# Performance work log

Measured on AMD Instinct MI355X. Metric: run time of the kernel, lower is better.

The kernel has to match this reference:

```python
import jax, jax.numpy as jnp
import numpy as np

N_ROOMS = 126          # len(building.rooms)
N = 2 + N_ROOMS        # state dim (reset_iv: 2 + n_rooms)
M = 1 + N_ROOMS        # input dim u = [Tout, Q_watts...]
T = 200000             # number of eval times
DT = 30.0              # seconds between eval points
TOUT_DT = 3600.0       # outside-temp table grid spacing (s)
K = 1700               # table length (covers 1000 + T*DT seconds)
LOAD_MAX = 500.0       # physical_loads_scaling: W/m^2 upper bound


def setup_inputs() -> dict:
    key = jax.random.key(0)
    ks = jax.random.split(key, 6)
    # Stable RC-style state matrix: negative diagonal dominates
    A = 1e-5 * jax.random.normal(ks[0], (N, N), dtype=jnp.float32) - 2e-4 * jnp.eye(N, dtype=jnp.float32)
    B = 1e-6 * jax.random.normal(ks[1], (N, M), dtype=jnp.float32)
    loads = jax.random.normal(ks[2], (2, N_ROOMS), dtype=jnp.float32)   # raw params (pre-sigmoid)
    areas = 10.0 + 40.0 * jax.random.uniform(ks[3], (N_ROOMS,), dtype=jnp.float32)  # room areas m^2
    Tout_vals = 10.0 + 5.0 * jax.random.normal(ks[4], (K,), dtype=jnp.float32)      # hourly Tout table
    t_eval = 1000.0 + DT * jnp.arange(T, dtype=jnp.float32)
    iv = 26.0 * jnp.ones((N, 1), dtype=jnp.float32)
    return {"A": A, "B": B, "loads": loads, "areas": areas,
            "Tout_vals": Tout_vals, "t_eval": t_eval, "iv": iv, "action": 1}


def _interp_tout(vals, t):
    # linear interpolation on a uniform grid starting at t=0 (replaces scipy interp1d)
    pos = t / TOUT_DT
    idx = jnp.clip(jnp.floor(pos).astype(jnp.int32), 0, K - 2)
    w = pos - idx.astype(pos.dtype)
    return vals[idx] * (1.0 - w) + vals[idx + 1] * w


def reference(A, B, loads, areas, Tout_vals, t_eval, iv, action):
    t0 = t_eval[0]
    ts = t_eval - t0
    # _build_loads: sigmoid transform + physical scaling
    lp = jax.nn.sigmoid(loads) * LOAD_MAX
    cool_load, gain_load = lp[0], lp[1]
    # f_ode constants: Q_area = -cool*action + gain; Q_watts = proportional_heating
    Q_watts = (-cool_load * action + gain_load) * areas        # [n_rooms]
    b_q = B[:, 1:] @ Q_watts                                   # [N] constant forcing
    b_T = B[:, 0]                                              # [N] Tout coupling
    x0 = iv[:, 0]

    def f(t, x):
        Tout = _interp_tout(Tout_vals, t + t0)
        return A @ x + b_T * Tout + b_q

    # torchdiffeq method='rk4' -> rk4_alt_step_func (3/8 rule)
    def step(x, tt):
        t, tn = tt
        dt = tn - t
        k1 = f(t, x)
        k2 = f(t + dt / 3.0, x + dt * k1 / 3.0)
        k3 = f(t + dt * 2.0 / 3.0, x + dt * (k2 - k1 / 3.0))
        k4 = f(t + dt, x + dt * (k1 - k2 + k3))
        xn = x + dt * (k1 + 3.0 * (k2 + k3) + k4) / 8.0
        return xn, xn

    _, traj = jax.lax.scan(step, x0, (ts[:-1], ts[1:]))
    out = jnp.concatenate([x0[None, :], traj], axis=0)         # [T, N]
    return out[..., None]                                      # [T, N, 1] matching iv shape
```

## Files before the change

### kernel.cpp

```cpp
#include <hip/hip_runtime.h>

#define N 128
#define NR 126
#define MBCOL 127
#define TSTEPS 200000
#define L1 49
#define C1 4096
#define L2 64
#define C2 64
#define KT 1700

#define OFF_Z     0
#define OFF_S     16384
#define OFF_P     32768
#define OFF_PW2   65536
#define OFF_PW4   81920
#define OFF_PW8   98304
#define OFF_PW16  114688
#define OFF_PW32  131072
#define OFF_Q     147456
#define OFF_WC    180224
#define OFF_ACC   212992
#define OFF_DELTA 737280
#define OFF_BQ    745472
#define OFF_BST   753664
#define OFF_PEH   65536
#define OFF_PEL   75776

typedef float v4f __attribute__((ext_vector_type(4)));
typedef __attribute__((ext_vector_type(8))) short bf16x8;
typedef __attribute__((ext_vector_type(4))) float f32x4;

#define LBAR() do { \
  __builtin_amdgcn_sched_barrier(0); \
  asm volatile("s_waitcnt lgkmcnt(0)" ::: "memory"); \
  __builtin_amdgcn_sched_barrier(0); \
  __builtin_amdgcn_s_barrier(); \
  __builtin_amdgcn_sched_barrier(0); \
} while (0)

#define GLD4(dst, p) \
  asm volatile("global_load_dwordx4 %0, %1, off" : "=v"(dst) : "v"(p))
#define PINQ(q) \
  asm volatile("s_waitcnt vmcnt(0)" \
    : "+v"(q[0]),"+v"(q[1]),"+v"(q[2]),"+v"(q[3]), \
      "+v"(q[4]),"+v"(q[5]),"+v"(q[6]),"+v"(q[7]), \
      "+v"(q[8]),"+v"(q[9]),"+v"(q[10]),"+v"(q[11]), \
      "+v"(q[12]),"+v"(q[13]),"+v"(q[14]),"+v"(q[15]))

__device__ __forceinline__ void loadQ16(v4f* qv, const float* pb)
{
  #pragma unroll
  for (int s = 0; s < 16; ++s) GLD4(qv[s], pb + 4*s);
  PINQ(qv);
}

__device__ __forceinline__ void bsplit(float f, unsigned short& h, unsigned short& l)
{
  unsigned int u = __float_as_uint(f);
  unsigned int r = (u + 0x7FFFu + ((u >> 16) & 1u)) >> 16;
  float hf = __uint_as_float(r << 16);
  h = (unsigned short)r;
  float lo = f - hf;
  unsigned int u2 = __float_as_uint(lo);
  unsigned int r2 = (u2 + 0x7FFFu + ((u2 >> 16) & 1u)) >> 16;
  l = (unsigned short)r2;
}

__global__ __launch_bounds__(128) void kPrep(
    const float* __restrict__ A, const float* __restrict__ B,
    const float* __restrict__ loads, const float* __restrict__ areas,
    const float* __restrict__ iv, const int* __restrict__ action,
    float* __restrict__ ws, float* __restrict__ out)
{
  __shared__ float qw[NR];
  __shared__ float ys[4][N];
  __shared__ float qs[4][N];
  int t = threadIdx.x;
  float actf = (float)action[0];
  if (t < NR) {
    float lc = (1.0f / (1.0f + expf(-loads[t]))) * 500.0f;
    float lg = (1.0f / (1.0f + expf(-loads[NR + t]))) * 500.0f;
    qw[t] = (-lc * actf + lg) * areas[t];
  }
  __syncthreads();
  {
    float bq = 0.0f;
    for (int i = 0; i < NR; ++i) bq += B[t * MBCOL + 1 + i] * qw[i];
    ys[0][t] = B[t * MBCOL];
    qs[0][t] = bq;
  }
  __syncthreads();
  for (int s = 1; s < 4; ++s) {
    float ay = 0.0f, aq = 0.0f;
    for (int k = 0; k < N; ++k) {
      float a = A[t * N + k];
      ay += a * ys[s-1][k];
      aq += a * qs[s-1][k];
    }
    ys[s][t] = 30.0f * ay;
    qs[s][t] = 30.0f * aq;
    __syncthreads();
  }
  float vs[5];
  vs[0] = 3.75f * (ys[0][t] + ys[1][t] + ys[2][t]*(1.0f/3.0f) + ys[3][t]*(1.0f/3.0f));
  vs[1] = 3.75f * (3.0f*ys[0][t] + 2.0f*ys[1][t] + ys[2][t]);
  vs[2] = 3.75f * (3.0f*ys[0][t] + ys[1][t]);
  vs[3] = 3.75f * ys[0][t];
  vs[4] = 3.75f * (8.0f*qs[0][t] + 4.0f*qs[1][t] + (4.0f/3.0f)*qs[2][t] + (1.0f/3.0f)*qs[3][t]);
  for (int m = 0; m < 5; ++m) ws[OFF_WC + (m*L1) * N + t] = vs[m];
  for (int i = t; i < N*N/4; i += 128) {
    float4 a = ((const float4*)A)[i];
    a.x *= 30.0f; a.y *= 30.0f; a.z *= 30.0f; a.w *= 30.0f;
    ((float4*)(ws + OFF_Z))[i] = a;
  }
  out[t] = iv[t];
}

__device__ __forceinline__ void mmRowR(const float* __restrict__ Aw,
                                       const float* __restrict__ Bw,
                                       float* __restrict__ Cw,
                                       float* __restrict__ Cw2,
                                       float* __restrict__ sm, int r)
{
  int t = threadIdx.x, c = t & 127, kh = t >> 7;
  const float* Ar = Aw + r*N + kh*64;
  const float* Bc = Bw + (kh*64)*N + c;
  float p0=0.f, p1=0.f, p2=0.f, p3=0.f;
  #pragma unroll 4
  for (int s = 0; s < 64; s += 4) {
    const float4 av = *(const float4*)(Ar + s);
    p0 = fmaf(av.x, Bc[(s+0)*N], p0);
    p1 = fmaf(av.y, Bc[(s+1)*N], p1);
    p2 = fmaf(av.z, Bc[(s+2)*N], p2);
    p3 = fmaf(av.w, Bc[(s+3)*N], p3);
  }
  sm[kh*128 + c] = (p0+p1)+(p2+p3);
  __syncthreads();
  if (kh == 0) {
    float v = sm[c] + sm[128 + c];
    Cw[r*N + c] = v;
    if (Cw2) Cw2[r*N + c] = v;
  }
}

__device__ __forceinline__ void polyRow(float* __restrict__ ws,
                                        float* __restrict__ sm)
{
  int t = threadIdx.x, c = t & 127, kh = t >> 7;
  int r = blockIdx.x;
  const float* Z = ws + OFF_Z;
  const float* S = ws + OFF_S;
  const float* Sr = S + r*N + kh*64;
  float x3=0.f, x4=0.f;
  #pragma unroll 4
  for (int s = 0; s < 64; s += 4) {
    const float4 av = *(const float4*)(Sr + s);
    int k = kh*64 + s;
    x3 = fmaf(av.x, Z[(k+0)*N+c], x3); x3 = fmaf(av.y, Z[(k+1)*N+c], x3);
    x3 = fmaf(av.z, Z[(k+2)*N+c], x3); x3 = fmaf(av.w, Z[(k+3)*N+c], x3);
    x4 = fmaf(av.x, S[(k+0)*N+c], x4); x4 = fmaf(av.y, S[(k+1)*N+c], x4);
    x4 = fmaf(av.z, S[(k+2)*N+c], x4); x4 = fmaf(av.w, S[(k+3)*N+c], x4);
  }
  sm[kh*128 + c] = x3;
  sm[256 + kh*128 + c] = x4;
  __syncthreads();
  if (kh == 0) {
    float a3 = sm[c] + sm[128+c];
    float a4 = sm[256+c] + sm[384+c];
    float pv = (r==c ? 1.0f : 0.0f) + Z[r*N+c] + 0.5f*S[r*N+c]
             + (1.0f/6.0f)*a3 + (1.0f/24.0f)*a4;
    ws[OFF_P + r*N + c] = pv;
  }
}

__device__ __forceinline__ void wUnit(const float* __restrict__ Pw,
                                      float* __restrict__ ws,
                                      int uw, int wbase, int wcount,
                                      float* __restrict__ wbuf )
{
  int t = threadIdx.x;
  int np = 5 * wcount;
  for (int i = t; i < 8*N; i += 256) {
    int pl = i >> 7, k = i & 127;
    int p = uw*8 + pl;
    float v = 0.0f;
    if (p < np) {
      int m = p / wcount, kk = p % wcount;
      v = ws[OFF_WC + (m*L1 + kk)*N + k];
    }
    wbuf[pl*N + k] = v;
  }
  __syncthreads();
  int r = t & 127, pg = t >> 7;
  float acc[4] = {0,0,0,0};
  #pragma unroll 2
  for (int k = 0; k < N; k += 4) {
    const float4 av = *(const float4*)(Pw + r*N + k);
    #pragma unroll
    for (int pi = 0; pi < 4; ++pi) {
      const float4 wv = *(const float4*)(wbuf + (pg*4+pi)*N + k);
      acc[pi] = fmaf(av.x, wv.x, acc[pi]);
      acc[pi] = fmaf(av.y, wv.y, acc[pi]);
      acc[pi] = fmaf(av.z, wv.z, acc[pi]);
      acc[pi] = fmaf(av.w, wv.w, acc[pi]);
    }
  }
  #pragma unroll
  for (int pi = 0; pi < 4; ++pi) {
    int p = uw*8 + pg*4 + pi;
    if (p < np) {
      int m = p / wcount, kk = p % wcount;
      ws[OFF_WC + (m*L1 + wbase + kk)*N + r] = acc[pi];
    }
  }
}

__global__ __launch_bounds__(256) void kPhase(float* __restrict__ ws, int ph)
{
  __shared__ float sm[1024];
  int b = blockIdx.x;
  if (ph == 1) { mmRowR(ws+OFF_Z, ws+OFF_Z, ws+OFF_S, nullptr, sm, b); return; }
  if (ph == 2) { polyRow(ws, sm); return; }
  if (ph <= 8) {
    int s = ph - 3;
    const int srcOff[6] = {OFF_P, OFF_PW2, OFF_PW4, OFF_PW8, OFF_PW16, OFF_PW32};
    const int dstOff[6] = {OFF_PW2, OFF_PW4, OFF_PW8, OFF_PW16, OFF_PW32, OFF_S};
    if (b < 128) {
      if (s < 5) mmRowR(ws+srcOff[s], ws+srcOff[s], ws+dstOff[s], nullptr, sm, b);
      else       mmRowR(ws+OFF_PW32, ws+OFF_PW16, ws+OFF_S, nullptr, sm, b);
    } else {
      int wbase  = (s < 5) ? (1 << s) : 32;
      int wcount = (s < 5) ? (1 << s) : 17;
      wUnit(ws + srcOff[s], ws, b - 128, wbase, wcount, sm);
    }
    return;
  }
  if (ph == 9) {
    if (b < 128) {
      mmRowR(ws+OFF_S, ws+OFF_P, ws+OFF_Z, ws+OFF_Q, sm, b);
    } else {
      int r = b - 128;
      int tt = threadIdx.x;
      if (tt < 160) {
        float val;
        if (tt < 128)      val = ws[OFF_P + r*N + tt];
        else if (tt < 133) val = ws[OFF_WC + ((tt-128)*L1)*N + r];
        else               val = 0.0f;
        unsigned short h, l2;
        bsplit(val, h, l2);
        ((unsigned short*)(ws + OFF_PEH))[r*160 + tt] = h;
        ((unsigned short*)(ws + OFF_PEL))[r*160 + tt] = l2;
      }
    }
    return;
  }
  {
    int d = ph - 8;
    const float* src = ws + ((d & 1) ? OFF_S : OFF_Z);
    float* dst       = ws + ((d & 1) ? OFF_Z : OFF_S);
    mmRowR(src, src, dst, nullptr, sm, b);
  }
}

__device__ __forceinline__ void build_table(float* lt, const float* __restrict__ Tout,
                                            int J0, int t, int cnt, int stride)
{
  int tbase = 1470*J0 + 1000;
  for (int s = t; s < cnt; s += stride) {
    float tt = (float)(tbase + 10*s);
    float pos = tt / 3600.0f;
    int idx = (int)pos;
    if (idx > KT-2) idx = KT-2;
    float w = pos - (float)idx;
    lt[s] = Tout[idx]*(1.0f-w) + Tout[idx+1]*w;
  }
}

__global__ __launch_bounds__(256) void k3_acc(const float* __restrict__ Tout,
                                              float* __restrict__ ws)
{
  __shared__ float lt[1184];
  int t = threadIdx.x;
  if (blockIdx.x >= 512) {
    mmRowR(ws+OFF_Z, ws+OFF_Z, ws+OFF_S, nullptr, lt, blockIdx.x - 512);
    return;
  }
  int J0 = blockIdx.x * 8;
  build_table(lt, Tout, J0, t, 1177, 256);
  __syncthreads();
  int r = t & 127, jh = t >> 7;
  float a[4] = {0.0f, 0.0f, 0.0f, 0.0f};
  for (int k = 0; k < L1; ++k) {
    float w0 = ws[OFF_WC + (0*L1+k)*N + r];
    float w1 = ws[OFF_WC + (1*L1+k)*N + r];
    float w2 = ws[OFF_WC + (2*L1+k)*N + r];
    float w3 = ws[OFF_WC + (3*L1+k)*N + r];
    float w4 = ws[OFF_WC + (4*L1+k)*N + r];
    #pragma unroll
    for (int q = 0; q < 4; ++q) {
      int cl = jh*4 + q;
      int soff = 3*(L1*cl + (L1-1) - k);
      a[q] += w0*lt[soff] + w1*lt[soff+1] + w2*lt[soff+2] + w3*lt[soff+3] + w4;
    }
  }
  #pragma unroll
  for (int q = 0; q < 4; ++q)
    ws[OFF_ACC + (size_t)(J0 + jh*4 + q)*N + r] = a[q];
}

__device__ __forceinline__ void mv_step3(const v4f* qv, float* x, float* ps,
                                         int r, int kh, float addv)
{
  const v4f* xp = (const v4f*)(x + kh*64);
  float p0=0.f, p1=0.f, p2=0.f, p3=0.f;
  #pragma unroll
  for (int s = 0; s < 16; s += 4) {
    v4f x0 = xp[s+0], x1 = xp[s+1], x2 = xp[s+2], x3 = xp[s+3];
    p0 = fmaf(qv[s+0][0],x0[0],p0); p0 = fmaf(qv[s+0][1],x0[1],p0);
    p0 = fmaf(qv[s+0][2],x0[2],p0); p0 = fmaf(qv[s+0][3],x0[3],p0);
    p1 = fmaf(qv[s+1][0],x1[0],p1); p1 = fmaf(qv[s+1][1],x1[1],p1);
    p1 = fmaf(qv[s+1][2],x1[2],p1); p1 = fmaf(qv[s+1][3],x1[3],p1);
    p2 = fmaf(qv[s+2][0],x2[0],p2); p2 = fmaf(qv[s+2][1],x2[1],p2);
    p2 = fmaf(qv[s+2][2],x2[2],p2); p2 = fmaf(qv[s+2][3],x2[3],p2);
    p3 = fmaf(qv[s+3][0],x3[0],p3); p3 = fmaf(qv[s+3][1],x3[1],p3);
    p3 = fmaf(qv[s+3][2],x3[2],p3); p3 = fmaf(qv[s+3][3],x3[3],p3);
  }
  ps[kh*128 + r] = (p0+p1)+(p2+p3);
  LBAR();
  if (kh == 0) x[r] = ps[r] + ps[128 + r] + addv;
  LBAR();
}

__global__ __launch_bounds__(256, 2) void k4_l2a(float* __restrict__ ws)
{
  __shared__ float x[N];
  __shared__ float ps[256];
  if (blockIdx.x >= 64) {
    mmRowR(ws+OFF_S, ws+OFF_S, ws+OFF_Z, nullptr, ps, blockIdx.x - 64);
    return;
  }
  int t = threadIdx.x, r = t & 127, kh = t >> 7;
  int q = blockIdx.x;
  v4f qv[16];
  loadQ16(qv, ws + OFF_Q + r*N + kh*64);
  if (t < N) x[t] = 0.0f;
  __syncthreads();
  float nxt = ws[OFF_ACC + (size_t)(q*L2)*N + r];
  for (int i = 0; i < L2; ++i) {
    float addv = nxt;
    if (i+1 < L2) nxt = ws[OFF_ACC + (size_t)(q*L2 + i+1)*N + r];
    mv_step3(qv, x, ps, r, kh, addv);
  }
  if (kh == 0) ws[OFF_DELTA + q*N + r] = x[r];
}

__global__ __launch_bounds__(256, 2) void k5_l3(const float* __restrict__ iv,
                                                float* __restrict__ ws)
{
  __shared__ float x[N];
  __shared__ float ps[256];
  __shared__ float dl[63*N];
  int t = threadIdx.x, r = t & 127, kh = t >> 7;
  v4f qv[16];
  loadQ16(qv, ws + OFF_Z + r*N + kh*64);
  for (int i = t; i < 63*N; i += 256) dl[i] = ws[OFF_DELTA + i];
  if (t < N) x[t] = iv[t];
  __syncthreads();
  for (int q = 0; q < C2; ++q) {
    if (kh == 0) ws[OFF_BQ + q*N + r] = x[r];
    if (q == C2-1) break;
    mv_step3(qv, x, ps, r, kh, dl[q*N + r]);
  }
}

__global__ __launch_bounds__(256, 2) void k6_l2b(float* __restrict__ ws)
{
  __shared__ float x[N];
  __shared__ float ps[256];
  int t = threadIdx.x, r = t & 127, kh = t >> 7;
  int q = blockIdx.x;
  v4f qv[16];
  loadQ16(qv, ws + OFF_Q + r*N + kh*64);
  if (t < N) x[t] = ws[OFF_BQ + q*N + t];
  __syncthreads();
  float nxt = ws[OFF_ACC + (size_t)(q*L2)*N + r];
  for (int i = 0; i < L2; ++i) {
    if (kh == 0) ws[OFF_BST + (size_t)(q*L2 + i)*N + r] = x[r];
    if (i == L2-1) break;
    float addv = nxt;
    nxt = ws[OFF_ACC + (size_t)(q*L2 + i+1)*N + r];
    mv_step3(qv, x, ps, r, kh, addv);
  }
}

__global__ __launch_bounds__(512) void k7_main(const float* __restrict__ Tout,
                                               const float* __restrict__ ws,
                                               float* __restrict__ out)
{
  __shared__ float ltp[3136];
  __shared__ __align__(16) unsigned short XbHi[16][168];
  __shared__ __align__(16) unsigned short XbLo[16][168];
  int t = threadIdx.x;
  int J0 = blockIdx.x * 16;

  for (int e = t; e < 3136; e += 512) {
    int cl = e / 196, rem = e - cl*196;
    int i = rem >> 2, m = rem & 3;
    float tt = (float)(1000 + 1470*(J0 + cl) + 30*i + 10*m);
    float pos = tt / 3600.0f;
    int idx = (int)pos;
    if (idx > KT-2) idx = KT-2;
    float w = pos - (float)idx;
    ltp[e] = Tout[idx]*(1.0f-w) + Tout[idx+1]*w;
  }
  for (int e = t; e < 2048; e += 512) {
    int cn = e >> 7, k = e & 127;
    unsigned short h, l2;
    bsplit(ws[OFF_BST + (size_t)(J0+cn)*N + k], h, l2);
    XbHi[cn][k] = h; XbLo[cn][k] = l2;
  }
  for (int e = t; e < 16*40; e += 512) {
    int cn = e / 40, k = 128 + (e - cn*40);
    XbHi[cn][k] = 0; XbLo[cn][k] = 0;
  }
  __syncthreads();
  if (t < 80) {
    int cn = t / 5, m = t - cn*5;
    float v = (m < 4) ? ltp[cn*196 + m] : 1.0f;
    unsigned short h, l2; bsplit(v, h, l2);
    XbHi[cn][128+m] = h; XbLo[cn][128+m] = l2;
  }

  int l = t & 63, w = t >> 6;
  int la = l & 15, lg = l >> 4;
  int rowA = w*16 + la;
  const unsigned short* peh = (const unsigned short*)(ws + OFF_PEH);
  const unsigned short* pel = (const unsigned short*)(ws + OFF_PEL);
  bf16x8 Ah[5], Al[5];
  #pragma unroll
  for (int kt = 0; kt < 5; ++kt) {
    Ah[kt] = *(const bf16x8*)(peh + rowA*160 + kt*32 + lg*8);
    Al[kt] = *(const bf16x8*)(pel + rowA*160 + kt*32 + lg*8);
  }
  __syncthreads();

  int rowD = w*16 + lg*4;
  int nnB = L1*(J0 + la);
  for (int i = 0; i < L1; ++i) {
    bf16x8 Bh[5], Bl[5];
    #pragma unroll
    for (int kt = 0; kt < 5; ++kt) {
      Bh[kt] = *(const bf16x8*)(&XbHi[la][kt*32 + lg*8]);
      Bl[kt] = *(const bf16x8*)(&XbLo[la][kt*32 + lg*8]);
    }
    f32x4 ahh = {0.f,0.f,0.f,0.f}, ahl = {0.f,0.f,0.f,0.f}, alh = {0.f,0.f,0.f,0.f};
    #pragma unroll
    for (int kt = 0; kt < 5; ++kt) {
      ahh = __builtin_amdgcn_mfma_f32_16x16x32_bf16(Ah[kt], Bh[kt], ahh, 0, 0, 0);
      ahl = __builtin_amdgcn_mfma_f32_16x16x32_bf16(Ah[kt], Bl[kt], ahl, 0, 0, 0);
      alh = __builtin_amdgcn_mfma_f32_16x16x32_bf16(Al[kt], Bh[kt], alh, 0, 0, 0);
    }
    f32x4 y = ahh + ahl + alh;
    int nn = nnB + i + 1;
    if (nn < TSTEPS)
      *(f32x4*)(out + (size_t)nn*N + rowD) = y;
    LBAR();
    unsigned short h0,h1,h2,h3,q0,q1,q2,q3;
    bsplit(y[0],h0,q0); bsplit(y[1],h1,q1); bsplit(y[2],h2,q2); bsplit(y[3],h3,q3);
    unsigned int hA = (unsigned)h0 | ((unsigned)h1<<16);
    unsigned int hB = (unsigned)h2 | ((unsigned)h3<<16);
    unsigned int lA = (unsigned)q0 | ((unsigned)q1<<16);
    unsigned int lB = (unsigned)q2 | ((unsigned)q3<<16);
    *reinterpret_cast<uint2*>(&XbHi[la][rowD]) = make_uint2(hA, hB);
    *reinterpret_cast<uint2*>(&XbLo[la][rowD]) = make_uint2(lA, lB);
    if (t < 64 && i < L1-1) {
      int cn = t >> 2, m = t & 3;
      float v = ltp[cn*196 + (i+1)*4 + m];
      unsigned short hh, ll; bsplit(v, hh, ll);
      XbHi[cn][128+m] = hh; XbLo[cn][128+m] = ll;
    }
    LBAR();
  }
}

extern "C" void kernel_launch(void* const* d_in, const int* in_sizes, int n_in,
                              void* d_out, int out_size, void* d_ws, size_t ws_size,
                              hipStream_t stream)
{
  const float* A     = (const float*)d_in[0];
  const float* B     = (const float*)d_in[1];
  const float* loads = (const float*)d_in[2];
  const float* areas = (const float*)d_in[3];
  const float* Tout  = (const float*)d_in[4];
  const float* iv    = (const float*)d_in[6];
  const int* action  = (const int*)d_in[7];
  float* out = (float*)d_out;
  float* ws  = (float*)d_ws;

  hipLaunchKernelGGL(kPrep, dim3(1), dim3(128), 0, stream,
                     A, B, loads, areas, iv, action, ws, out);
  const int phGrid[10] = {0, 128, 128, 129, 130, 131, 133, 138, 139, 256};
  for (int ph = 1; ph <= 9; ++ph)
    hipLaunchKernelGGL(kPhase, dim3(phGrid[ph]), dim3(256), 0, stream, ws, ph);
  hipLaunchKernelGGL(k3_acc,  dim3(640),  dim3(256), 0, stream, Tout, ws);
  hipLaunchKernelGGL(k4_l2a,  dim3(192),  dim3(256), 0, stream, ws);
  for (int ph = 10; ph <= 13; ++ph)
    hipLaunchKernelGGL(kPhase, dim3(128), dim3(256), 0, stream, ws, ph);
  hipLaunchKernelGGL(k5_l3,   dim3(1),    dim3(256), 0, stream, iv, ws);
  hipLaunchKernelGGL(k6_l2b,  dim3(64),   dim3(256), 0, stream, ws);
  hipLaunchKernelGGL(k7_main, dim3(256),  dim3(512), 0, stream, Tout, ws, out);
}
```

Before: 252.0 us.

## Replace serial chunk-level scans with parallel tree reduction over block forcing

Replaces the two-level sequential scan (64-step per-chunk accumulation, then 63-step serial combine) with a log-depth tree of matrix-vector combine passes that fold pairs of chunk forcings using successive powers of the propagator. The matrix powers are computed alongside in the same launches. The remaining serial scans shrink to 15 steps at the top level and 15 steps at the second level, and the finest 16-step level moves into the main kernel's prologue. This shortens the serial critical path but adds more kernel launches and extra workspace traffic.

```diff
diff --git a/kernel.cpp b/kernel.cpp
--- a/kernel.cpp
+++ b/kernel.cpp
@@ -6,8 +6,6 @@
 #define TSTEPS 200000
 #define L1 49
 #define C1 4096
-#define L2 64
-#define C2 64
 #define KT 1700
 
 #define OFF_Z     0
@@ -22,14 +20,24 @@
 #define OFF_WC    180224
 #define OFF_ACC   212992
 #define OFF_DELTA 737280
-#define OFF_BQ    745472
-#define OFF_BST   753664
-#define OFF_PEH   65536
-#define OFF_PEL   75776
+#define OFF_B1    753664
+#define OFF_B2    1015808
+#define OFF_B3    1146880
+#define OFF_A16   1212416
+#define OFF_C1    1245184
+#define OFF_C2    1261568
+#define OFF_C3    1269760
+#define OFF_A256  1273856
+#define OFF_BQ256 1275904
+#define OFF_BST16 753664
+#define OFF_Q256  786432
 
 typedef float v4f __attribute__((ext_vector_type(4)));
 typedef __attribute__((ext_vector_type(8))) short bf16x8;
 typedef __attribute__((ext_vector_type(4))) float f32x4;
+
+#define OFF_PEH   65536
+#define OFF_PEL   75776
 
 #define LBAR() do { \
   __builtin_amdgcn_sched_barrier(0); \
@@ -47,6 +55,10 @@
       "+v"(q[4]),"+v"(q[5]),"+v"(q[6]),"+v"(q[7]), \
       "+v"(q[8]),"+v"(q[9]),"+v"(q[10]),"+v"(q[11]), \
       "+v"(q[12]),"+v"(q[13]),"+v"(q[14]),"+v"(q[15]))
+#define PINQ8(q) \
+  asm volatile("s_waitcnt vmcnt(0)" \
+    : "+v"(q[0]),"+v"(q[1]),"+v"(q[2]),"+v"(q[3]), \
+      "+v"(q[4]),"+v"(q[5]),"+v"(q[6]),"+v"(q[7]))
 
 __device__ __forceinline__ void loadQ16(v4f* qv, const float* pb)
 {
@@ -216,10 +228,55 @@
   }
 }
 
+__device__ __forceinline__ void treeUnit(const float* __restrict__ Qm,
+                                         const float* __restrict__ src,
+                                         float* __restrict__ dst,
+                                         int uw, float* __restrict__ wbuf)
+{
+  int t = threadIdx.x;
+  for (int i = t; i < 8*N; i += 256) {
+    int pl = i >> 7, k = i & 127;
+    wbuf[pl*N + k] = src[(size_t)(2*(uw*8 + pl))*N + k];
+  }
+  __syncthreads();
+  int r = t & 127, pg = t >> 7;
+  float acc[4] = {0,0,0,0};
+  #pragma unroll 2
+  for (int k = 0; k < N; k += 4) {
+    const float4 av = *(const float4*)(Qm + r*N + k);
+    #pragma unroll
+    for (int pi = 0; pi < 4; ++pi) {
+      const float4 wv = *(const float4*)(wbuf + (pg*4+pi)*N + k);
+      acc[pi] = fmaf(av.x, wv.x, acc[pi]);
+      acc[pi] = fmaf(av.y, wv.y, acc[pi]);
+      acc[pi] = fmaf(av.z, wv.z, acc[pi]);
+      acc[pi] = fmaf(av.w, wv.w, acc[pi]);
+    }
+  }
+  #pragma unroll
+  for (int pi = 0; pi < 4; ++pi) {
+    int j = uw*8 + pg*4 + pi;
+    dst[(size_t)j*N + r] = acc[pi] + src[(size_t)(2*j + 1)*N + r];
+  }
+}
+
 __global__ __launch_bounds__(256) void kPhase(float* __restrict__ ws, int ph)
 {
   __shared__ float sm[1024];
   int b = blockIdx.x;
+  if (ph >= 20) {
+    int lv = ph - 20;
+    const int srcO[8] = {OFF_ACC, OFF_B1, OFF_B2, OFF_B3, OFF_A16, OFF_C1, OFF_C2, OFF_C3};
+    const int dstO[8] = {OFF_B1, OFF_B2, OFF_B3, OFF_A16, OFF_C1, OFF_C2, OFF_C3, OFF_A256};
+    const int nco[8]  = {2048, 1024, 512, 256, 128, 64, 32, 16};
+    const int qO[8]   = {OFF_Q, OFF_S, OFF_P, OFF_PW8, OFF_PW16, OFF_PW32, OFF_Z, OFF_DELTA};
+    const int pS[8]   = {OFF_S, OFF_P, OFF_PW8, OFF_PW16, OFF_PW32, OFF_Z, OFF_DELTA, -1};
+    const int pD[8]   = {OFF_P, OFF_PW8, OFF_PW16, OFF_PW32, OFF_Z, OFF_DELTA, OFF_Q256, -1};
+    int nb = nco[lv] >> 3;
+    if (b < nb) treeUnit(ws + qO[lv], ws + srcO[lv], ws + dstO[lv], b, sm);
+    else if (pS[lv] >= 0) mmRowR(ws + pS[lv], ws + pS[lv], ws + pD[lv], nullptr, sm, b - nb);
+    return;
+  }
   if (ph == 1) { mmRowR(ws+OFF_Z, ws+OFF_Z, ws+OFF_S, nullptr, sm, b); return; }
   if (ph == 2) { polyRow(ws, sm); return; }
   if (ph <= 8) {
@@ -255,12 +312,6 @@
     }
     return;
   }
-  {
-    int d = ph - 8;
-    const float* src = ws + ((d & 1) ? OFF_S : OFF_Z);
-    float* dst       = ws + ((d & 1) ? OFF_Z : OFF_S);
-    mmRowR(src, src, dst, nullptr, sm, b);
-  }
 }
 
 __device__ __forceinline__ void build_table(float* lt, const float* __restrict__ Tout,
@@ -332,65 +383,41 @@
   LBAR();
 }
 
-__global__ __launch_bounds__(256, 2) void k4_l2a(float* __restrict__ ws)
+__global__ __launch_bounds__(256, 2) void k5a_l3(const float* __restrict__ iv,
+                                                 float* __restrict__ ws)
 {
   __shared__ float x[N];
   __shared__ float ps[256];
-  if (blockIdx.x >= 64) {
-    mmRowR(ws+OFF_S, ws+OFF_S, ws+OFF_Z, nullptr, ps, blockIdx.x - 64);
-    return;
-  }
+  __shared__ float dl[15*N];
   int t = threadIdx.x, r = t & 127, kh = t >> 7;
-  int q = blockIdx.x;
   v4f qv[16];
-  loadQ16(qv, ws + OFF_Q + r*N + kh*64);
-  if (t < N) x[t] = 0.0f;
-  __syncthreads();
-  float nxt = ws[OFF_ACC + (size_t)(q*L2)*N + r];
-  for (int i = 0; i < L2; ++i) {
-    float addv = nxt;
-    if (i+1 < L2) nxt = ws[OFF_ACC + (size_t)(q*L2 + i+1)*N + r];
-    mv_step3(qv, x, ps, r, kh, addv);
-  }
-  if (kh == 0) ws[OFF_DELTA + q*N + r] = x[r];
-}
-
-__global__ __launch_bounds__(256, 2) void k5_l3(const float* __restrict__ iv,
-                                                float* __restrict__ ws)
+  loadQ16(qv, ws + OFF_Q256 + r*N + kh*64);
+  for (int i = t; i < 15*N; i += 256) dl[i] = ws[OFF_A256 + i];
+  if (t < N) x[t] = iv[t];
+  __syncthreads();
+  for (int p = 0; p < 16; ++p) {
+    if (kh == 0) ws[OFF_BQ256 + p*N + r] = x[r];
+    if (p == 15) break;
+    mv_step3(qv, x, ps, r, kh, dl[p*N + r]);
+  }
+}
+
+__global__ __launch_bounds__(256, 2) void k5b_l2(float* __restrict__ ws)
 {
   __shared__ float x[N];
   __shared__ float ps[256];
-  __shared__ float dl[63*N];
+  __shared__ float dl[15*N];
   int t = threadIdx.x, r = t & 127, kh = t >> 7;
+  int p = blockIdx.x;
   v4f qv[16];
-  loadQ16(qv, ws + OFF_Z + r*N + kh*64);
-  for (int i = t; i < 63*N; i += 256) dl[i] = ws[OFF_DELTA + i];
-  if (t < N) x[t] = iv[t];
-  __syncthreads();
-  for (int q = 0; q < C2; ++q) {
-    if (kh == 0) ws[OFF_BQ + q*N + r] = x[r];
-    if (q == C2-1) break;
-    mv_step3(qv, x, ps, r, kh, dl[q*N + r]);
-  }
-}
-
-__global__ __launch_bounds__(256, 2) void k6_l2b(float* __restrict__ ws)
-{
-  __shared__ float x[N];
-  __shared__ float ps[256];
-  int t = threadIdx.x, r = t & 127, kh = t >> 7;
-  int q = blockIdx.x;
-  v4f qv[16];
-  loadQ16(qv, ws + OFF_Q + r*N + kh*64);
-  if (t < N) x[t] = ws[OFF_BQ + q*N + t];
-  __syncthreads();
-  float nxt = ws[OFF_ACC + (size_t)(q*L2)*N + r];
-  for (int i = 0; i < L2; ++i) {
-    if (kh == 0) ws[OFF_BST + (size_t)(q*L2 + i)*N + r] = x[r];
-    if (i == L2-1) break;
-    float addv = nxt;
-    nxt = ws[OFF_ACC + (size_t)(q*L2 + i+1)*N + r];
-    mv_step3(qv, x, ps, r, kh, addv);
+  loadQ16(qv, ws + OFF_PW16 + r*N + kh*64);
+  for (int i = t; i < 15*N; i += 256) dl[i] = ws[OFF_A16 + (size_t)p*15*0 + (size_t)(p*16)*N + i];
+  if (t < N) x[t] = ws[OFF_BQ256 + p*N + t];
+  __syncthreads();
+  for (int i = 0; i < 16; ++i) {
+    if (kh == 0) ws[OFF_BST16 + (size_t)(p*16 + i)*N + r] = x[r];
+    if (i == 15) break;
+    mv_step3(qv, x, ps, r, kh, dl[i*N + r]);
   }
 }
 
@@ -401,35 +428,66 @@
   __shared__ float ltp[3136];
   __shared__ __align__(16) unsigned short XbHi[16][168];
   __shared__ __align__(16) unsigned short XbLo[16][168];
+  __shared__ float xf[N];
+  __shared__ float psf[512];
   int t = threadIdx.x;
-  int J0 = blockIdx.x * 16;
+  int m = blockIdx.x;
+  int J0 = m * 16;
 
   for (int e = t; e < 3136; e += 512) {
     int cl = e / 196, rem = e - cl*196;
-    int i = rem >> 2, m = rem & 3;
-    float tt = (float)(1000 + 1470*(J0 + cl) + 30*i + 10*m);
+    int i = rem >> 2, mm = rem & 3;
+    float tt = (float)(1000 + 1470*(J0 + cl) + 30*i + 10*mm);
     float pos = tt / 3600.0f;
     int idx = (int)pos;
     if (idx > KT-2) idx = KT-2;
     float w = pos - (float)idx;
     ltp[e] = Tout[idx]*(1.0f-w) + Tout[idx+1]*w;
   }
-  for (int e = t; e < 2048; e += 512) {
-    int cn = e >> 7, k = e & 127;
-    unsigned short h, l2;
-    bsplit(ws[OFF_BST + (size_t)(J0+cn)*N + k], h, l2);
-    XbHi[cn][k] = h; XbLo[cn][k] = l2;
-  }
   for (int e = t; e < 16*40; e += 512) {
     int cn = e / 40, k = 128 + (e - cn*40);
     XbHi[cn][k] = 0; XbLo[cn][k] = 0;
   }
   __syncthreads();
   if (t < 80) {
-    int cn = t / 5, m = t - cn*5;
-    float v = (m < 4) ? ltp[cn*196 + m] : 1.0f;
+    int cn = t / 5, mm = t - cn*5;
+    float v = (mm < 4) ? ltp[cn*196 + mm] : 1.0f;
     unsigned short h, l2; bsplit(v, h, l2);
-    XbHi[cn][128+m] = h; XbLo[cn][128+m] = l2;
+    XbHi[cn][128+mm] = h; XbLo[cn][128+mm] = l2;
+  }
+
+  int r = t & 127, kq = t >> 7;
+  v4f q8[8];
+  #pragma unroll
+  for (int s = 0; s < 8; ++s) GLD4(q8[s], ws + OFF_Q + r*N + kq*32 + 4*s);
+  PINQ8(q8);
+  if (t < N) xf[t] = ws[OFF_BST16 + (size_t)m*N + t];
+  __syncthreads();
+  float nxtA = (t < N) ? ws[OFF_ACC + (size_t)(J0)*N + t] : 0.0f;
+  for (int c = 0; c < 16; ++c) {
+    if (t < N) {
+      unsigned short h, l2; bsplit(xf[t], h, l2);
+      XbHi[c][t] = h; XbLo[c][t] = l2;
+    }
+    if (c == 15) { LBAR(); break; }
+    float pp0 = 0.f, pp1 = 0.f;
+    const v4f* xp = (const v4f*)(xf + kq*32);
+    #pragma unroll
+    for (int s = 0; s < 8; s += 2) {
+      v4f x0 = xp[s], x1 = xp[s+1];
+      pp0 = fmaf(q8[s][0],x0[0],pp0);   pp0 = fmaf(q8[s][1],x0[1],pp0);
+      pp0 = fmaf(q8[s][2],x0[2],pp0);   pp0 = fmaf(q8[s][3],x0[3],pp0);
+      pp1 = fmaf(q8[s+1][0],x1[0],pp1); pp1 = fmaf(q8[s+1][1],x1[1],pp1);
+      pp1 = fmaf(q8[s+1][2],x1[2],pp1); pp1 = fmaf(q8[s+1][3],x1[3],pp1);
+    }
+    psf[t] = pp0 + pp1;
+    LBAR();
+    if (t < N) {
+      float addv = nxtA;
+      nxtA = ws[OFF_ACC + (size_t)(J0 + c + 1)*N + t];
+      xf[t] = psf[t] + psf[t+128] + psf[t+256] + psf[t+384] + addv;
+    }
+    LBAR();
   }
 
   int l = t & 63, w = t >> 6;
@@ -443,7 +501,6 @@
     Ah[kt] = *(const bf16x8*)(peh + rowA*160 + kt*32 + lg*8);
     Al[kt] = *(const bf16x8*)(pel + rowA*160 + kt*32 + lg*8);
   }
-  __syncthreads();
 
   int rowD = w*16 + lg*4;
   int nnB = L1*(J0 + la);
@@ -475,10 +532,10 @@
     *reinterpret_cast<uint2*>(&XbHi[la][rowD]) = make_uint2(hA, hB);
     *reinterpret_cast<uint2*>(&XbLo[la][rowD]) = make_uint2(lA, lB);
     if (t < 64 && i < L1-1) {
-      int cn = t >> 2, m = t & 3;
-      float v = ltp[cn*196 + (i+1)*4 + m];
+      int cn = t >> 2, mm = t & 3;
+      float v = ltp[cn*196 + (i+1)*4 + mm];
       unsigned short hh, ll; bsplit(v, hh, ll);
-      XbHi[cn][128+m] = hh; XbLo[cn][128+m] = ll;
+      XbHi[cn][128+mm] = hh; XbLo[cn][128+mm] = ll;
     }
     LBAR();
   }
@@ -503,11 +560,11 @@
   const int phGrid[10] = {0, 128, 128, 129, 130, 131, 133, 138, 139, 256};
   for (int ph = 1; ph <= 9; ++ph)
     hipLaunchKernelGGL(kPhase, dim3(phGrid[ph]), dim3(256), 0, stream, ws, ph);
-  hipLaunchKernelGGL(k3_acc,  dim3(640),  dim3(256), 0, stream, Tout, ws);
-  hipLaunchKernelGGL(k4_l2a,  dim3(192),  dim3(256), 0, stream, ws);
-  for (int ph = 10; ph <= 13; ++ph)
-    hipLaunchKernelGGL(kPhase, dim3(128), dim3(256), 0, stream, ws, ph);
-  hipLaunchKernelGGL(k5_l3,   dim3(1),    dim3(256), 0, stream, iv, ws);
-  hipLaunchKernelGGL(k6_l2b,  dim3(64),   dim3(256), 0, stream, ws);
-  hipLaunchKernelGGL(k7_main, dim3(256),  dim3(512), 0, stream, Tout, ws, out);
-}
+  hipLaunchKernelGGL(k3_acc, dim3(640), dim3(256), 0, stream, Tout, ws);
+  const int trGrid[8] = {384, 256, 192, 160, 144, 136, 132, 2};
+  for (int lv = 0; lv < 8; ++lv)
+    hipLaunchKernelGGL(kPhase, dim3(trGrid[lv]), dim3(256), 0, stream, ws, 20 + lv);
+  hipLaunchKernelGGL(k5a_l3, dim3(1),   dim3(256), 0, stream, iv, ws);
+  hipLaunchKernelGGL(k5b_l2, dim3(16),  dim3(256), 0, stream, ws);
+  hipLaunchKernelGGL(k7_main, dim3(256), dim3(512), 0, stream, Tout, ws, out);
+}
```

Measured after the change: 228.4 us. -9.4%, faster.
